# Kernel tuning notes

Hardware: AMD Instinct MI355X
Metric: run time of the kernel (lower is better)

Reference implementation:

```python
import jax, jax.numpy as jnp
import numpy as np

B, C, IN, H = 64, 128, 1024, 512  # batch, channels, input features (=='seq_length' arg), hidden


def setup_inputs() -> dict:
    key = jax.random.key(0)
    ks = jax.random.split(key, 9)
    s = 1.0 / np.sqrt(H)  # PyTorch LSTM init: U(-1/sqrt(H), 1/sqrt(H))
    u = lambda k, shape: jax.random.uniform(k, shape, jnp.float32, -s, s)
    return {
        "x": jax.random.normal(ks[0], (B, C, IN), jnp.float32),
        # layer 0: one weight set per direction (fwd, bwd)
        "W_ih0": u(ks[1], (2, 4 * H, IN)),
        "W_hh0": u(ks[2], (2, 4 * H, H)),
        "b_ih0": u(ks[3], (2, 4 * H)),
        "b_hh0": u(ks[4], (2, 4 * H)),
        # layers 1..2: input is concat of both directions (2H)
        "W_ih12": u(ks[5], (2, 2, 4 * H, 2 * H)),
        "W_hh12": u(ks[6], (2, 2, 4 * H, H)),
        "b_ih12": u(ks[7], (2, 2, 4 * H)),
        "b_hh12": u(ks[8], (2, 2, 4 * H)),
    }


def _cell(inp, W_ih, b_ih, b_hh):
    # One LSTM step from zero state (h0 = c0 = 0): W_hh @ h0 == 0, f*c0 == 0.
    gates = inp @ W_ih.T + b_ih + b_hh  # [N, 4H]
    i, f, g, o = jnp.split(gates, 4, axis=-1)  # PyTorch gate order: i, f, g, o
    c = jax.nn.sigmoid(i) * jnp.tanh(g)
    return jax.nn.sigmoid(o) * jnp.tanh(c)  # h, shape [N, H]


def reference(x, W_ih0, W_hh0, b_ih0, b_hh0, W_ih12, W_hh12, b_ih12, b_hh12):
    b, c, n = x.shape
    # Each channel is an independent seq-len-1 LSTM call with zero init state,
    # so fold channels into the batch dimension. W_hh* contribute nothing (h0=0).
    xb = x.reshape(b * c, n)
    h = jnp.concatenate(
        [_cell(xb, W_ih0[d], b_ih0[d], b_hh0[d]) for d in range(2)], axis=-1
    )  # [b*c, 2H]
    for l in range(2):  # layers 1 and 2
        h = jnp.concatenate(
            [_cell(h, W_ih12[l, d], b_ih12[l, d], b_hh12[l, d]) for d in range(2)],
            axis=-1,
        )
    return h.reshape(b, c, 2 * H)  # [batch, channels, 2*hidden]
```

## Files before the change

### kernel.cpp

```cpp
#include <hip/hip_runtime.h>


typedef float f32x4 __attribute__((ext_vector_type(4)));
typedef short short8 __attribute__((ext_vector_type(8)));
typedef unsigned short u16;

#define NP 3072
#define MROWS 8192
#define KDIM 1024
#define BM 128
#define BN 96
#define BK 32
#define LDS_TILE 14336

__device__ __forceinline__ u16 f2bf(float f) {
  unsigned u = __float_as_uint(f);
  u += 0x7fffu + ((u >> 16) & 1u);
  return (u16)(u >> 16);
}
__device__ __forceinline__ float sigmoid_f(float x) {
  return 1.0f / (1.0f + __expf(-x));
}
__device__ __forceinline__ float tanh_f(float x) {
  float xc = fminf(fmaxf(x, -15.0f), 15.0f);
  float e = __expf(2.0f * xc);
  return (e - 1.0f) / (e + 1.0f);
}
__device__ __forceinline__ void gload_lds16(const void* g, void* l) {
  __builtin_amdgcn_global_load_lds((const __attribute__((address_space(1))) void*)g,
                                   (__attribute__((address_space(3))) void*)l,
                                   16, 0, 0);
}


__global__ __launch_bounds__(256) void k_convert_x(const float* __restrict__ x,
                                                   u16* __restrict__ out) {
  int tid = blockIdx.x * 256 + threadIdx.x;
  const float4* src = (const float4*)x + (size_t)tid * 2;
  float4 v0 = src[0], v1 = src[1];
  union { u16 u[8]; uint4 v; } r;
  r.u[0] = f2bf(v0.x); r.u[1] = f2bf(v0.y); r.u[2] = f2bf(v0.z); r.u[3] = f2bf(v0.w);
  r.u[4] = f2bf(v1.x); r.u[5] = f2bf(v1.y); r.u[6] = f2bf(v1.z); r.u[7] = f2bf(v1.w);
  ((uint4*)out)[tid] = r.v;
}

__global__ __launch_bounds__(256) void k_pack_w(const float* __restrict__ Wih0,
                                                const float* __restrict__ Wih12,
                                                u16* __restrict__ P) {
  int tid = blockIdx.x * 256 + threadIdx.x;
  int s   = tid / (NP * 128);
  int rem = tid - s * (NP * 128);
  int p   = rem >> 7;
  int k8  = rem & 127;
  int hb = p / 48;
  int pr = p - hb * 48;
  int gs = pr >> 4;
  int hl = pr & 15;
  int hcol = hb * 16 + hl;
  int dir = hcol >> 9;
  int h   = hcol & 511;
  int og  = (gs == 0) ? 0 : (gs + 1);
  const float* src;
  if (s == 0)
    src = Wih0 + ((size_t)(dir * 2048 + og * 512 + h)) * 1024 + k8 * 8;
  else
    src = Wih12 + ((size_t)(((s - 1) * 2 + dir) * 2048 + og * 512 + h)) * 1024 + k8 * 8;
  float4 v0 = ((const float4*)src)[0];
  float4 v1 = ((const float4*)src)[1];
  union { u16 u[8]; uint4 v; } r;
  r.u[0] = f2bf(v0.x); r.u[1] = f2bf(v0.y); r.u[2] = f2bf(v0.z); r.u[3] = f2bf(v0.w);
  r.u[4] = f2bf(v1.x); r.u[5] = f2bf(v1.y); r.u[6] = f2bf(v1.z); r.u[7] = f2bf(v1.w);
  ((uint4*)P)[tid] = r.v;
}

__global__ __launch_bounds__(256) void k_pack_bias(const float* __restrict__ bih0,
                                                   const float* __restrict__ bhh0,
                                                   const float* __restrict__ bih12,
                                                   const float* __restrict__ bhh12,
                                                   float* __restrict__ pb) {
  int tid = blockIdx.x * 256 + threadIdx.x;
  if (tid >= 3 * NP) return;
  int s = tid / NP;
  int p = tid - s * NP;
  int hb = p / 48;
  int pr = p - hb * 48;
  int gs = pr >> 4;
  int hl = pr & 15;
  int hcol = hb * 16 + hl;
  int dir = hcol >> 9;
  int h   = hcol & 511;
  int og  = (gs == 0) ? 0 : (gs + 1);
  int j   = og * 512 + h;
  float v;
  if (s == 0) {
    int i = dir * 2048 + j;
    v = bih0[i] + bhh0[i];
  } else {
    int i = ((s - 1) * 2 + dir) * 2048 + j;
    v = bih12[i] + bhh12[i];
  }
  pb[tid] = v;
}


#define BAR()    __builtin_amdgcn_s_barrier()
#define SCHEDB() __builtin_amdgcn_sched_barrier(0)
#define WAITV(N) asm volatile("s_waitcnt vmcnt(" #N ")" ::: "memory")
#define MM(Macc, Aop, Bop) Macc = __builtin_amdgcn_mfma_f32_16x16x32_bf16(Aop, Bop, Macc, 0, 0, 0)

#define STAGE(BUF, KT) \
  gload_lds16(srcA + (size_t)(KT) * BK,              lds + (BUF) * LDS_TILE + t * 16); \
  gload_lds16(srcA + 64 * KDIM + (size_t)(KT) * BK,  lds + (BUF) * LDS_TILE + 4096 + t * 16); \
  gload_lds16(srcB + (size_t)(KT) * BK,              lds + (BUF) * LDS_TILE + 8192 + t * 16); \
  if (t < 128) { gload_lds16(srcB + 64 * KDIM + (size_t)(KT) * BK, lds + (BUF) * LDS_TILE + 12288 + t * 16); }

#define KSTEP(RBUF, SBUF, KT, DOST, LASTT) \
  { \
    if (DOST) { STAGE(SBUF, (KT) + 2); } \
    const char* base = lds + (RBUF) * LDS_TILE; \
    short8 a0 = *(const short8*)(base + aOff); \
    short8 a1 = *(const short8*)(base + aOff + 1024); \
    short8 a2 = *(const short8*)(base + aOff + 2048); \
    short8 a3 = *(const short8*)(base + aOff + 3072); \
    short8 b0 = *(const short8*)(base + bOff); \
    short8 b1 = *(const short8*)(base + bOff + 1024); \
    short8 b2 = *(const short8*)(base + bOff + 2048); \
    __builtin_amdgcn_s_setprio(1); \
    MM(acc[0][0], a0, b0); MM(acc[1][0], a1, b0); MM(acc[2][0], a2, b0); MM(acc[3][0], a3, b0); \
    MM(acc[0][1], a0, b1); MM(acc[1][1], a1, b1); MM(acc[2][1], a2, b1); MM(acc[3][1], a3, b1); \
    MM(acc[0][2], a0, b2); MM(acc[1][2], a1, b2); MM(acc[2][2], a2, b2); MM(acc[3][2], a3, b2); \
    __builtin_amdgcn_s_setprio(0); \
    if (DOST) { if (t < 128) { WAITV(4); } else { WAITV(3); } } \
    else if (!(LASTT)) { WAITV(0); } \
    if (!(LASTT)) { BAR(); SCHEDB(); } \
  }

template <bool F32OUT>
__global__ __launch_bounds__(256, 3) void k_lstm_gemm97(const u16* __restrict__ A,
                                                        const u16* __restrict__ Bp,
                                                        const float* __restrict__ bias,
                                                        void* __restrict__ outp) {
  __shared__ __align__(16) char lds[3 * LDS_TILE];
  const int t    = threadIdx.x;
  const int lane = t & 63;
  const int w    = t >> 6;
  const int wr   = w >> 1;
  const int wc   = w & 1;
  const int r16  = lane & 15, kg = lane >> 4;

  const int n_hw = blockIdx.y * gridDim.x + blockIdx.x;
  const int c    = n_hw & 7;
  const int wlc  = n_hw >> 3;
  const int bx   = (c & 1) * 16 + (wlc & 15);
  const int by   = (c >> 1) * 16 + (wlc >> 4);
  const int brow = by * BM;
  const int bn0  = bx * BN;

  const int sw   = (r16 >> 1) & 3;
  const int slot = (kg ^ sw) << 4;
  const int aOff = wr * 4096 + r16 * 64 + slot;
  const int bOff = 8192 + wc * 3072 + r16 * 64 + slot;

  const int srow = t >> 2;
  const int koct = ((t & 3) ^ ((t >> 3) & 3)) << 3;
  const u16* srcA = A  + (size_t)(brow + srow) * KDIM + koct;
  const u16* srcB = Bp + (size_t)(bn0  + srow) * KDIM + koct;

  f32x4 acc[4][3];
#pragma unroll
  for (int m = 0; m < 4; ++m)
#pragma unroll
    for (int n = 0; n < 3; ++n) acc[m][n] = (f32x4){0.f, 0.f, 0.f, 0.f};

  STAGE(0, 0);
  STAGE(1, 1);
  if (t < 128) { WAITV(4); } else { WAITV(3); }
  BAR(); SCHEDB();

  for (int k3 = 0; k3 < 10; ++k3) {
    int kt = k3 * 3;
    KSTEP(0, 2, kt + 0, 1, 0);
    KSTEP(1, 0, kt + 1, 1, 0);
    KSTEP(2, 1, kt + 2, 1, 0);
  }
  KSTEP(0, 0, 30, 0, 0);
  KSTEP(1, 0, 31, 0, 1);

  {
    int pbase = bn0 + wc * 48;
    float biV = bias[pbase + r16];
    float bgV = bias[pbase + 16 + r16];
    float boV = bias[pbase + 32 + r16];
    int hcol = (2 * bx + wc) * 16 + r16;
#pragma unroll
    for (int m = 0; m < 4; ++m) {
      int rowb = brow + wr * 64 + m * 16 + kg * 4;
#pragma unroll
      for (int r = 0; r < 4; ++r) {
        float vi = acc[m][0][r] + biV;
        float vg = acc[m][1][r] + bgV;
        float vo = acc[m][2][r] + boV;
        float c2 = sigmoid_f(vi) * tanh_f(vg);
        float hv = sigmoid_f(vo) * tanh_f(c2);
        size_t oidx = (size_t)(rowb + r) * 1024 + hcol;
        if (F32OUT) ((float*)outp)[oidx] = hv;
        else        ((u16*)outp)[oidx]   = f2bf(hv);
      }
    }
  }
}

extern "C" void kernel_launch(void* const* d_in, const int* in_sizes, int n_in,
                              void* d_out, int out_size, void* d_ws, size_t ws_size,
                              hipStream_t stream) {
  const float* x     = (const float*)d_in[0];
  const float* Wih0  = (const float*)d_in[1];
  const float* bih0  = (const float*)d_in[3];
  const float* bhh0  = (const float*)d_in[4];
  const float* Wih12 = (const float*)d_in[5];
  const float* bih12 = (const float*)d_in[7];
  const float* bhh12 = (const float*)d_in[8];

  char* ws = (char*)d_ws;
  u16*   xbf = (u16*)ws;
  u16*   h1  = (u16*)(ws + 16777216);
  u16*   h2  = (u16*)(ws + 33554432);
  u16*   P3  = (u16*)(ws + 50331648);
  float* pb3 = (float*)(ws + 69206016);

  k_convert_x<<<4096, 256, 0, stream>>>(x, xbf);
  k_pack_w<<<4608, 256, 0, stream>>>(Wih0, Wih12, P3);
  k_pack_bias<<<36, 256, 0, stream>>>(bih0, bhh0, bih12, bhh12, pb3);

  dim3 grid(NP / BN, MROWS / BM);
  k_lstm_gemm97<false><<<grid, 256, 0, stream>>>(xbf, P3, pb3, h1);
  k_lstm_gemm97<false><<<grid, 256, 0, stream>>>(h1, P3 + (size_t)NP * KDIM, pb3 + NP, h2);
  k_lstm_gemm97<true ><<<grid, 256, 0, stream>>>(h2, P3 + (size_t)2 * NP * KDIM, pb3 + 2 * NP, d_out);
}
```

Baseline: 232.2 us.

## Enlarge GEMM tiles to 256x384 with 512-thread blocks and 8x6 per-wave accumulators

Raises the block tile from 128x96 to 256x384 and the block size to 512 threads (8 waves in a 2x4 grid), so each wave holds 8x6 MFMA accumulators and reuses each A fragment across six B fragments. LDS staging is rebuilt so every thread issues five 16-byte global-to-LDS loads per K step, and the block swizzle is remapped for the smaller 8x32 grid. The aim is more arithmetic per LDS and global byte and less redundant reloading of A and W. In exchange it uses far more registers and about 120KB of LDS per block, lowers occupancy, and leaves only 256 blocks to spread across the CUs.

```diff
diff --git a/kernel.cpp b/kernel.cpp
--- a/kernel.cpp
+++ b/kernel.cpp
@@ -8,10 +8,10 @@
 #define NP 3072
 #define MROWS 8192
 #define KDIM 1024
-#define BM 128
-#define BN 96
+#define BM 256
+#define BN 384
 #define BK 32
-#define LDS_TILE 14336
+#define LDS_TILE 40960
 
 __device__ __forceinline__ u16 f2bf(float f) {
   unsigned u = __float_as_uint(f);
@@ -109,72 +109,91 @@
 #define MM(Macc, Aop, Bop) Macc = __builtin_amdgcn_mfma_f32_16x16x32_bf16(Aop, Bop, Macc, 0, 0, 0)
 
 #define STAGE(BUF, KT) \
-  gload_lds16(srcA + (size_t)(KT) * BK,              lds + (BUF) * LDS_TILE + t * 16); \
-  gload_lds16(srcA + 64 * KDIM + (size_t)(KT) * BK,  lds + (BUF) * LDS_TILE + 4096 + t * 16); \
-  gload_lds16(srcB + (size_t)(KT) * BK,              lds + (BUF) * LDS_TILE + 8192 + t * 16); \
-  if (t < 128) { gload_lds16(srcB + 64 * KDIM + (size_t)(KT) * BK, lds + (BUF) * LDS_TILE + 12288 + t * 16); }
+  { char* dst = lds + (BUF) * LDS_TILE + t * 16; \
+    gload_lds16(srcA + (size_t)(KT) * BK,               dst); \
+    gload_lds16(srcA + 128 * KDIM + (size_t)(KT) * BK,  dst + 8192); \
+    gload_lds16(srcB + (size_t)(KT) * BK,               dst + 16384); \
+    gload_lds16(srcB + 128 * KDIM + (size_t)(KT) * BK,  dst + 24576); \
+    gload_lds16(srcB + 256 * KDIM + (size_t)(KT) * BK,  dst + 32768); }
 
 #define KSTEP(RBUF, SBUF, KT, DOST, LASTT) \
   { \
     if (DOST) { STAGE(SBUF, (KT) + 2); } \
     const char* base = lds + (RBUF) * LDS_TILE; \
-    short8 a0 = *(const short8*)(base + aOff); \
-    short8 a1 = *(const short8*)(base + aOff + 1024); \
-    short8 a2 = *(const short8*)(base + aOff + 2048); \
-    short8 a3 = *(const short8*)(base + aOff + 3072); \
-    short8 b0 = *(const short8*)(base + bOff); \
-    short8 b1 = *(const short8*)(base + bOff + 1024); \
-    short8 b2 = *(const short8*)(base + bOff + 2048); \
+    short8 a0 = *(const short8*)(base + aBase); \
+    short8 a1 = *(const short8*)(base + aBase + 1024); \
+    short8 a2 = *(const short8*)(base + aBase + 2048); \
+    short8 a3 = *(const short8*)(base + aBase + 3072); \
+    short8 a4 = *(const short8*)(base + aBase + 4096); \
+    short8 a5 = *(const short8*)(base + aBase + 5120); \
+    short8 a6 = *(const short8*)(base + aBase + 6144); \
+    short8 a7 = *(const short8*)(base + aBase + 7168); \
+    short8 b0 = *(const short8*)(base + bBase); \
+    short8 b1 = *(const short8*)(base + bBase + 1024); \
+    short8 b2 = *(const short8*)(base + bBase + 2048); \
     __builtin_amdgcn_s_setprio(1); \
     MM(acc[0][0], a0, b0); MM(acc[1][0], a1, b0); MM(acc[2][0], a2, b0); MM(acc[3][0], a3, b0); \
+    MM(acc[4][0], a4, b0); MM(acc[5][0], a5, b0); MM(acc[6][0], a6, b0); MM(acc[7][0], a7, b0); \
     MM(acc[0][1], a0, b1); MM(acc[1][1], a1, b1); MM(acc[2][1], a2, b1); MM(acc[3][1], a3, b1); \
+    MM(acc[4][1], a4, b1); MM(acc[5][1], a5, b1); MM(acc[6][1], a6, b1); MM(acc[7][1], a7, b1); \
     MM(acc[0][2], a0, b2); MM(acc[1][2], a1, b2); MM(acc[2][2], a2, b2); MM(acc[3][2], a3, b2); \
+    MM(acc[4][2], a4, b2); MM(acc[5][2], a5, b2); MM(acc[6][2], a6, b2); MM(acc[7][2], a7, b2); \
     __builtin_amdgcn_s_setprio(0); \
-    if (DOST) { if (t < 128) { WAITV(4); } else { WAITV(3); } } \
+    b0 = *(const short8*)(base + bBase + 3072); \
+    b1 = *(const short8*)(base + bBase + 4096); \
+    b2 = *(const short8*)(base + bBase + 5120); \
+    __builtin_amdgcn_s_setprio(1); \
+    MM(acc[0][3], a0, b0); MM(acc[1][3], a1, b0); MM(acc[2][3], a2, b0); MM(acc[3][3], a3, b0); \
+    MM(acc[4][3], a4, b0); MM(acc[5][3], a5, b0); MM(acc[6][3], a6, b0); MM(acc[7][3], a7, b0); \
+    MM(acc[0][4], a0, b1); MM(acc[1][4], a1, b1); MM(acc[2][4], a2, b1); MM(acc[3][4], a3, b1); \
+    MM(acc[4][4], a4, b1); MM(acc[5][4], a5, b1); MM(acc[6][4], a6, b1); MM(acc[7][4], a7, b1); \
+    MM(acc[0][5], a0, b2); MM(acc[1][5], a1, b2); MM(acc[2][5], a2, b2); MM(acc[3][5], a3, b2); \
+    MM(acc[4][5], a4, b2); MM(acc[5][5], a5, b2); MM(acc[6][5], a6, b2); MM(acc[7][5], a7, b2); \
+    __builtin_amdgcn_s_setprio(0); \
+    if (DOST) { WAITV(5); } \
     else if (!(LASTT)) { WAITV(0); } \
     if (!(LASTT)) { BAR(); SCHEDB(); } \
   }
 
 template <bool F32OUT>
-__global__ __launch_bounds__(256, 3) void k_lstm_gemm97(const u16* __restrict__ A,
-                                                        const u16* __restrict__ Bp,
-                                                        const float* __restrict__ bias,
-                                                        void* __restrict__ outp) {
+__global__ __launch_bounds__(512, 2) void k_lstm_gemmW(const u16* __restrict__ A,
+                                                       const u16* __restrict__ Bp,
+                                                       const float* __restrict__ bias,
+                                                       void* __restrict__ outp) {
   __shared__ __align__(16) char lds[3 * LDS_TILE];
   const int t    = threadIdx.x;
   const int lane = t & 63;
   const int w    = t >> 6;
-  const int wr   = w >> 1;
-  const int wc   = w & 1;
+  const int wr   = w >> 2;
+  const int wc   = w & 3;
   const int r16  = lane & 15, kg = lane >> 4;
 
   const int n_hw = blockIdx.y * gridDim.x + blockIdx.x;
   const int c    = n_hw & 7;
   const int wlc  = n_hw >> 3;
-  const int bx   = (c & 1) * 16 + (wlc & 15);
-  const int by   = (c >> 1) * 16 + (wlc >> 4);
+  const int bx   = (c & 1) * 4 + (wlc & 3);
+  const int by   = (c >> 1) * 8 + (wlc >> 2);
   const int brow = by * BM;
   const int bn0  = bx * BN;
 
-  const int sw   = (r16 >> 1) & 3;
-  const int slot = (kg ^ sw) << 4;
-  const int aOff = wr * 4096 + r16 * 64 + slot;
-  const int bOff = 8192 + wc * 3072 + r16 * 64 + slot;
+  const int slot = (kg ^ ((r16 >> 1) & 3)) << 4;
+  const int aBase = wr * 8192 + r16 * 64 + slot;
+  const int bBase = 16384 + wc * 6144 + r16 * 64 + slot;
 
   const int srow = t >> 2;
   const int koct = ((t & 3) ^ ((t >> 3) & 3)) << 3;
   const u16* srcA = A  + (size_t)(brow + srow) * KDIM + koct;
   const u16* srcB = Bp + (size_t)(bn0  + srow) * KDIM + koct;
 
-  f32x4 acc[4][3];
-#pragma unroll
-  for (int m = 0; m < 4; ++m)
-#pragma unroll
-    for (int n = 0; n < 3; ++n) acc[m][n] = (f32x4){0.f, 0.f, 0.f, 0.f};
+  f32x4 acc[8][6];
+#pragma unroll
+  for (int m = 0; m < 8; ++m)
+#pragma unroll
+    for (int n = 0; n < 6; ++n) acc[m][n] = (f32x4){0.f, 0.f, 0.f, 0.f};
 
   STAGE(0, 0);
   STAGE(1, 1);
-  if (t < 128) { WAITV(4); } else { WAITV(3); }
+  WAITV(5);
   BAR(); SCHEDB();
 
   for (int k3 = 0; k3 < 10; ++k3) {
@@ -186,20 +205,21 @@
   KSTEP(0, 0, 30, 0, 0);
   KSTEP(1, 0, 31, 0, 1);
 
-  {
-    int pbase = bn0 + wc * 48;
+#pragma unroll
+  for (int trio = 0; trio < 2; ++trio) {
+    int pbase = bn0 + wc * 96 + trio * 48;
     float biV = bias[pbase + r16];
     float bgV = bias[pbase + 16 + r16];
     float boV = bias[pbase + 32 + r16];
-    int hcol = (2 * bx + wc) * 16 + r16;
-#pragma unroll
-    for (int m = 0; m < 4; ++m) {
-      int rowb = brow + wr * 64 + m * 16 + kg * 4;
+    int hcol = (bx * 8 + wc * 2 + trio) * 16 + r16;
+#pragma unroll
+    for (int m = 0; m < 8; ++m) {
+      int rowb = brow + wr * 128 + m * 16 + kg * 4;
 #pragma unroll
       for (int r = 0; r < 4; ++r) {
-        float vi = acc[m][0][r] + biV;
-        float vg = acc[m][1][r] + bgV;
-        float vo = acc[m][2][r] + boV;
+        float vi = acc[m][trio * 3 + 0][r] + biV;
+        float vg = acc[m][trio * 3 + 1][r] + bgV;
+        float vo = acc[m][trio * 3 + 2][r] + boV;
         float c2 = sigmoid_f(vi) * tanh_f(vg);
         float hv = sigmoid_f(vo) * tanh_f(c2);
         size_t oidx = (size_t)(rowb + r) * 1024 + hcol;
@@ -233,7 +253,7 @@
   k_pack_bias<<<36, 256, 0, stream>>>(bih0, bhh0, bih12, bhh12, pb3);
 
   dim3 grid(NP / BN, MROWS / BM);
-  k_lstm_gemm97<false><<<grid, 256, 0, stream>>>(xbf, P3, pb3, h1);
-  k_lstm_gemm97<false><<<grid, 256, 0, stream>>>(h1, P3 + (size_t)NP * KDIM, pb3 + NP, h2);
-  k_lstm_gemm97<true ><<<grid, 256, 0, stream>>>(h2, P3 + (size_t)2 * NP * KDIM, pb3 + 2 * NP, d_out);
-}
+  k_lstm_gemmW<false><<<grid, 512, 0, stream>>>(xbf, P3, pb3, h1);
+  k_lstm_gemmW<false><<<grid, 512, 0, stream>>>(h1, P3 + (size_t)NP * KDIM, pb3 + NP, h2);
+  k_lstm_gemmW<true ><<<grid, 512, 0, stream>>>(h2, P3 + (size_t)2 * NP * KDIM, pb3 + 2 * NP, d_out);
+}
```

New measurement: 198.0 us. -14.7%, faster.
